# Kernel optimization log

Measured on AMD Instinct MI355X. Metric: run time of the kernel, lower is better.

Reference implementation:

```python
import jax, jax.numpy as jnp
import numpy as np

B, S, DIM, NH, HD = 2, 2048, 4096, 32, 128  # head_dim = dim // n_kv_heads
ROPE_THETA = 10000.0


def _apply_rope(xh, cos, sin):
    # xh: (B, S, H, HD); cos/sin: (S, HD//2). Llama interleaved-pair rotation
    # (view head_dim as complex pairs, multiply by e^{i*theta}).
    b, s, h, d = xh.shape
    xp = xh.reshape(b, s, h, d // 2, 2)
    x0, x1 = xp[..., 0], xp[..., 1]
    c = cos[None, :, None, :]
    sn = sin[None, :, None, :]
    o0 = x0 * c - x1 * sn
    o1 = x0 * sn + x1 * c
    return jnp.stack([o0, o1], axis=-1).reshape(b, s, h, d)


def setup_inputs() -> dict:
    key = jax.random.key(0)
    ks = jax.random.split(key, 5)
    scale = 1.0 / np.sqrt(DIM)
    x = jax.random.normal(ks[0], (B, S, DIM), dtype=jnp.float32)
    wq = jax.random.normal(ks[1], (DIM, DIM), dtype=jnp.float32) * scale
    wk = jax.random.normal(ks[2], (DIM, DIM), dtype=jnp.float32) * scale
    wv = jax.random.normal(ks[3], (DIM, DIM), dtype=jnp.float32) * scale
    wo = jax.random.normal(ks[4], (DIM, DIM), dtype=jnp.float32) * scale
    # precomputed rotary table (real/imag of freqs_cis)
    t = jnp.arange(S, dtype=jnp.float32)
    inv_freq = 1.0 / (ROPE_THETA ** (jnp.arange(0, HD, 2, dtype=jnp.float32) / HD))
    ang = t[:, None] * inv_freq[None, :]  # (S, HD//2)
    freqs_cos, freqs_sin = jnp.cos(ang), jnp.sin(ang)
    # additive causal mask
    i = jnp.arange(S)
    mask = jnp.where(i[None, :] <= i[:, None], 0.0, -jnp.inf).astype(jnp.float32)
    return {"x": x, "wq": wq, "wk": wk, "wv": wv, "wo": wo,
            "freqs_cos": freqs_cos, "freqs_sin": freqs_sin,
            "mask": mask, "start_pos": 0}


def reference(x, wq, wk, wv, wo, freqs_cos, freqs_sin, mask, start_pos):
    bsz, seqlen, dim = x.shape
    # nn.Linear(bias=False): y = x @ W^T
    xq = (x @ wq.T).reshape(bsz, seqlen, NH, HD)
    xk = (x @ wk.T).reshape(bsz, seqlen, NH, HD)
    xv = (x @ wv.T).reshape(bsz, seqlen, NH, HD)
    xq = _apply_rope(xq, freqs_cos, freqs_sin)
    xk = _apply_rope(xk, freqs_cos, freqs_sin)
    # training path: keys/values = current xk/xv (no cache)
    scores = jnp.einsum('bqhd,bkhd->bhqk', xq, xk) / np.sqrt(HD)
    scores = scores + mask[None, None, :, :]
    probs = jax.nn.softmax(scores.astype(jnp.float32), axis=-1).astype(x.dtype)
    out = jnp.einsum('bhqk,bkhd->bqhd', probs, xv).reshape(bsz, seqlen, dim)
    return out @ wo.T
```

## Files before the change

kernel.cpp:

```cpp
#include <hip/hip_runtime.h>

typedef __bf16 bf16;
typedef __attribute__((ext_vector_type(8))) __bf16 bf16x8;
typedef __attribute__((ext_vector_type(4))) float f32x4;

#define MFMA_BF16(a,b,c) __builtin_amdgcn_mfma_f32_16x16x32_bf16((a),(b),(c),0,0,0)

__device__ __forceinline__ void gld_lds16(const void* g, void* l) {
  __builtin_amdgcn_global_load_lds(
      (__attribute__((address_space(1))) void*)(g),
      (__attribute__((address_space(3))) void*)(l), 16, 0, 0);
}

__device__ __forceinline__ bf16x8 cvt8(float4 u, float4 v) {
  bf16x8 r;
  r[0] = (bf16)u.x; r[1] = (bf16)u.y; r[2] = (bf16)u.z; r[3] = (bf16)u.w;
  r[4] = (bf16)v.x; r[5] = (bf16)v.y; r[6] = (bf16)v.z; r[7] = (bf16)v.w;
  return r;
}

__global__ __launch_bounds__(256) void fill_kernel(float* p, int n, float v) {
  int i = blockIdx.x * 256 + threadIdx.x;
  if (i < n) p[i] = v;
}

__global__ __launch_bounds__(256) void cvt_kernel(const float* __restrict__ s, bf16* __restrict__ d) {
  size_t i = ((size_t)blockIdx.x * 256 + threadIdx.x) * 4;
  float4 a = *(const float4*)(s + i);
  ushort4 r;
  r.x = __builtin_bit_cast(unsigned short, (bf16)a.x);
  r.y = __builtin_bit_cast(unsigned short, (bf16)a.y);
  r.z = __builtin_bit_cast(unsigned short, (bf16)a.z);
  r.w = __builtin_bit_cast(unsigned short, (bf16)a.w);
  *(ushort4*)(d + i) = r;
}


template<int IH, int KS>
__device__ __forceinline__ void mfma_phase(const char* rb, int sA, int sB,
                                           f32x4 (&acc)[8][4], bf16x8 (&bq)[4])
{
  bf16x8 afr[4];
#pragma unroll
  for (int i2 = 0; i2 < 4; ++i2)
    afr[i2] = *(const bf16x8*)(rb + KS * 16384 + sA + (IH * 4 + i2) * 1024);
  if (IH == 0) {
#pragma unroll
    for (int j = 0; j < 4; ++j)
      bq[j] = *(const bf16x8*)(rb + 32768 + KS * 16384 + sB + j * 1024);
  }
  __builtin_amdgcn_s_barrier();
  __builtin_amdgcn_s_setprio(1);
#pragma unroll
  for (int i2 = 0; i2 < 4; ++i2)
#pragma unroll
    for (int j = 0; j < 4; ++j)
      acc[IH * 4 + i2][j] = MFMA_BF16(afr[i2], bq[j], acc[IH * 4 + i2][j]);
  __builtin_amdgcn_s_setprio(0);
}

__device__ __forceinline__ void gemm256_core(
    const bf16* __restrict__ Ag, const bf16* __restrict__ Wg,
    char* smem, int m0, int n0, f32x4 (&acc)[8][4])
{
  constexpr int NT = 64;
  const int tid = threadIdx.x;
  const int lane = tid & 63;
  const int l15 = lane & 15, quad = lane >> 4;
  const int wave = tid >> 6;
  const int wm = wave >> 2, wn = wave & 3;

  const int swz = (((l15 & 1) * 4 + quad) ^ (l15 >> 1));
  const int sA = ((wm * 64 + (l15 >> 1)) * 8 + swz) * 16;
  const int sB = ((wn * 32 + (l15 >> 1)) * 8 + swz) * 16;

  int r0, c0, r1, c1;
  { int s = tid;       int rp = s >> 3, y = (s & 7) ^ (rp & 7); r0 = rp * 2 + (y >> 2); c0 = y & 3; }
  { int s = 512 + tid; int rp = s >> 3, y = (s & 7) ^ (rp & 7); r1 = rp * 2 + (y >> 2); c1 = y & 3; }

  const bf16* gA0 = Ag + (size_t)(m0 + r0) * 4096 + c0 * 8;
  const bf16* gA1 = Ag + (size_t)(m0 + r1) * 4096 + c1 * 8;
  const bf16* gB0 = Wg + (size_t)(n0 + r0) * 4096 + c0 * 8;
  const bf16* gB1 = Wg + (size_t)(n0 + r1) * 4096 + c1 * 8;

  const int d0 = tid * 16, d1 = (512 + tid) * 16;

#pragma unroll
  for (int i = 0; i < 8; i++)
#pragma unroll
    for (int j = 0; j < 4; j++) acc[i][j] = (f32x4){0.f, 0.f, 0.f, 0.f};

  gld_lds16(gA0,      smem + d0);          gld_lds16(gA1,      smem + d1);
  gld_lds16(gB0,      smem + 32768 + d0);  gld_lds16(gB1,      smem + 32768 + d1);
  gld_lds16(gA0 + 32, smem + 16384 + d0);  gld_lds16(gA1 + 32, smem + 16384 + d1);
  gld_lds16(gB0 + 32, smem + 49152 + d0);  gld_lds16(gB1 + 32, smem + 49152 + d1);

#pragma unroll 2
  for (int t = 0; t < NT; ++t) {
    const int p = t & 1;
    const char* rb = smem + p * 65536;
    char* wb = smem + (p ^ 1) * 65536;
    const int kn = (t + 1) * 64;
    const bool st = (t + 1 < NT);

    asm volatile("s_waitcnt vmcnt(4)" ::: "memory");
    __builtin_amdgcn_s_barrier();

    bf16x8 bq0[4];
    if (st) { gld_lds16(gA0 + kn, wb + d0); gld_lds16(gA1 + kn, wb + d1); }
    mfma_phase<0, 0>(rb, sA, sB, acc, bq0);
    __builtin_amdgcn_s_barrier();

    if (st) { gld_lds16(gB0 + kn, wb + 32768 + d0); gld_lds16(gB1 + kn, wb + 32768 + d1); }
    mfma_phase<1, 0>(rb, sA, sB, acc, bq0);

    if (st) asm volatile("s_waitcnt vmcnt(4)" ::: "memory");
    else    asm volatile("s_waitcnt vmcnt(0)" ::: "memory");
    __builtin_amdgcn_s_barrier();

    bf16x8 bq1[4];
    if (st) { gld_lds16(gA0 + kn + 32, wb + 16384 + d0); gld_lds16(gA1 + kn + 32, wb + 16384 + d1); }
    mfma_phase<0, 1>(rb, sA, sB, acc, bq1);
    __builtin_amdgcn_s_barrier();

    if (st) { gld_lds16(gB0 + kn + 32, wb + 49152 + d0); gld_lds16(gB1 + kn + 32, wb + 49152 + d1); }
    mfma_phase<1, 1>(rb, sA, sB, acc, bq1);
  }
}

__global__ __launch_bounds__(512) void gemm256_qkv(
    const bf16* __restrict__ A,
    const bf16* __restrict__ W0, const bf16* __restrict__ W1, const bf16* __restrict__ W2,
    bf16* __restrict__ C0, bf16* __restrict__ C1, bf16* __restrict__ C2)
{
  __shared__ __align__(16) char smem[131072];
  const int z = blockIdx.z;
  const bf16* __restrict__ W = (z == 0) ? W0 : ((z == 1) ? W1 : W2);
  bf16* __restrict__ C = (z == 0) ? C0 : ((z == 1) ? C1 : C2);

  const int bid = blockIdx.x;
  const int swb = (bid & 7) * 32 + (bid >> 3);
  const int m0 = (swb & 15) << 8;
  const int n0 = (swb >> 4) << 8;

  f32x4 acc[8][4];
  gemm256_core(A, W, smem, m0, n0, acc);

  const int tid = threadIdx.x, lane = tid & 63, wave = tid >> 6;
  const int l15 = lane & 15, quad = lane >> 4;
  const int wm = wave >> 2, wn = wave & 3;

  if (z == 2) {
#pragma unroll
    for (int i = 0; i < 8; i++) {
      const int mg = m0 + wm * 128 + i * 16 + quad * 4;
      const int bb = mg >> 11, ss = mg & 2047;
#pragma unroll
      for (int j = 0; j < 4; j++) {
        const int n = n0 + wn * 64 + j * 16 + l15;
        ushort4 pk;
        pk.x = __builtin_bit_cast(unsigned short, (bf16)acc[i][j][0]);
        pk.y = __builtin_bit_cast(unsigned short, (bf16)acc[i][j][1]);
        pk.z = __builtin_bit_cast(unsigned short, (bf16)acc[i][j][2]);
        pk.w = __builtin_bit_cast(unsigned short, (bf16)acc[i][j][3]);
        *(ushort4*)&C[((size_t)bb * 4096 + n) * 2048 + ss] = pk;
      }
    }
  } else {
#pragma unroll
    for (int i = 0; i < 8; i++) {
      const int row = m0 + wm * 128 + i * 16 + quad * 4;
#pragma unroll
      for (int j = 0; j < 4; j++) {
        const int col = n0 + wn * 64 + j * 16 + l15;
#pragma unroll
        for (int r = 0; r < 4; r++)
          C[(size_t)(row + r) * 4096 + col] = (bf16)acc[i][j][r];
      }
    }
  }
}

__global__ __launch_bounds__(512) void gemm256_out(
    const bf16* __restrict__ A, const bf16* __restrict__ W, float* __restrict__ C)
{
  __shared__ __align__(16) char smem[131072];
  const int bid = blockIdx.x;
  const int swb = (bid & 7) * 32 + (bid >> 3);
  const int m0 = (swb & 15) << 8;
  const int n0 = (swb >> 4) << 8;

  f32x4 acc[8][4];
  gemm256_core(A, W, smem, m0, n0, acc);

  const int tid = threadIdx.x, lane = tid & 63, wave = tid >> 6;
  const int l15 = lane & 15, quad = lane >> 4;
  const int wm = wave >> 2, wn = wave & 3;

#pragma unroll
  for (int i = 0; i < 8; i++) {
    const int row = m0 + wm * 128 + i * 16 + quad * 4;
#pragma unroll
    for (int j = 0; j < 4; j++) {
      const int col = n0 + wn * 64 + j * 16 + l15;
#pragma unroll
      for (int r = 0; r < 4; r++)
        C[(size_t)(row + r) * 4096 + col] = acc[i][j][r];
    }
  }
}

__global__ __launch_bounds__(256) void gemm_f32in(
    const float* __restrict__ A,
    const float* __restrict__ W0, const float* __restrict__ W1, const float* __restrict__ W2,
    bf16* __restrict__ C0, bf16* __restrict__ C1, bf16* __restrict__ C2)
{
  constexpr int K = 4096, N = 4096;
  __shared__ __align__(16) bf16 As[128 * 32];
  __shared__ __align__(16) bf16 Bs[128 * 32];
  const int z = blockIdx.z;
  const float* __restrict__ W = (z == 0) ? W0 : ((z == 1) ? W1 : W2);
  bf16* __restrict__ C = (z == 0) ? C0 : ((z == 1) ? C1 : C2);
  const int tid = threadIdx.x;
  const int lane = tid & 63, wave = tid >> 6;
  const int l15 = lane & 15, quad = lane >> 4;
  const int m0 = blockIdx.x * 128, n0 = blockIdx.y * 128;
  const int wm = (wave & 1) * 64, wn = (wave >> 1) * 64;

  const int srow = tid >> 2;
  const int scol = (tid & 3) * 8;
  const float* gA = A + (size_t)(m0 + srow) * K + scol;
  const float* gW = W + (size_t)(n0 + srow) * K + scol;
  bf16* lA = &As[srow * 32 + scol];
  bf16* lB = &Bs[srow * 32 + scol];

  f32x4 acc[4][4];
#pragma unroll
  for (int i = 0; i < 4; i++)
#pragma unroll
    for (int j = 0; j < 4; j++) acc[i][j] = (f32x4){0.f, 0.f, 0.f, 0.f};

  for (int k0 = 0; k0 < K; k0 += 32) {
    float4 a0 = *(const float4*)(gA + k0);
    float4 a1 = *(const float4*)(gA + k0 + 4);
    float4 a2 = *(const float4*)(gA + k0 + (size_t)64 * K);
    float4 a3 = *(const float4*)(gA + k0 + (size_t)64 * K + 4);
    float4 b0 = *(const float4*)(gW + k0);
    float4 b1 = *(const float4*)(gW + k0 + 4);
    float4 b2 = *(const float4*)(gW + k0 + (size_t)64 * K);
    float4 b3 = *(const float4*)(gW + k0 + (size_t)64 * K + 4);
    __syncthreads();
    *(bf16x8*)lA              = cvt8(a0, a1);
    *(bf16x8*)(lA + 64 * 32)  = cvt8(a2, a3);
    *(bf16x8*)lB              = cvt8(b0, b1);
    *(bf16x8*)(lB + 64 * 32)  = cvt8(b2, b3);
    __syncthreads();
    bf16x8 af[4], bfr[4];
#pragma unroll
    for (int i = 0; i < 4; i++) af[i]  = *(const bf16x8*)&As[(wm + i * 16 + l15) * 32 + quad * 8];
#pragma unroll
    for (int j = 0; j < 4; j++) bfr[j] = *(const bf16x8*)&Bs[(wn + j * 16 + l15) * 32 + quad * 8];
#pragma unroll
    for (int i = 0; i < 4; i++)
#pragma unroll
      for (int j = 0; j < 4; j++)
        acc[i][j] = MFMA_BF16(af[i], bfr[j], acc[i][j]);
  }

  if (z == 2) {
#pragma unroll
    for (int i = 0; i < 4; i++) {
      const int mg = m0 + wm + i * 16 + quad * 4;
      const int bb = mg >> 11, ss = mg & 2047;
#pragma unroll
      for (int j = 0; j < 4; j++) {
        const int n = n0 + wn + j * 16 + l15;
        ushort4 pk;
        pk.x = __builtin_bit_cast(unsigned short, (bf16)acc[i][j][0]);
        pk.y = __builtin_bit_cast(unsigned short, (bf16)acc[i][j][1]);
        pk.z = __builtin_bit_cast(unsigned short, (bf16)acc[i][j][2]);
        pk.w = __builtin_bit_cast(unsigned short, (bf16)acc[i][j][3]);
        *(ushort4*)&C[((size_t)bb * 4096 + n) * 2048 + ss] = pk;
      }
    }
  } else {
#pragma unroll
    for (int i = 0; i < 4; i++) {
      const int row = m0 + wm + i * 16 + quad * 4;
#pragma unroll
      for (int j = 0; j < 4; j++) {
        const int col = n0 + wn + j * 16 + l15;
#pragma unroll
        for (int r = 0; r < 4; r++)
          C[(size_t)(row + r) * N + col] = (bf16)acc[i][j][r];
      }
    }
  }
}

__global__ __launch_bounds__(256) void rope_kernel(
    bf16* __restrict__ q, bf16* __restrict__ kk,
    const float* __restrict__ fc, const float* __restrict__ fs)
{
  const int t = blockIdx.x * 256 + threadIdx.x;
  const int i4 = (t & 15) << 2;
  const int row = t >> 4;
  const int s = (row >> 5) & 2047;

  float4 c4 = *(const float4*)(fc + s * 64 + i4);
  float4 s4 = *(const float4*)(fs + s * 64 + i4);
  float c[4]  = {c4.x, c4.y, c4.z, c4.w};
  float sn[4] = {s4.x, s4.y, s4.z, s4.w};

  const int off = row * 128 + (i4 << 1);
  uint4 qv = *(const uint4*)(q + off);
  uint4 kv = *(const uint4*)(kk + off);
  unsigned qa[4] = {qv.x, qv.y, qv.z, qv.w};
  unsigned ka[4] = {kv.x, kv.y, kv.z, kv.w};
#pragma unroll
  for (int p = 0; p < 4; p++) {
    float x0 = __builtin_bit_cast(float, (qa[p] & 0xffffu) << 16);
    float x1 = __builtin_bit_cast(float, (qa[p] >> 16) << 16);
    unsigned lo = __builtin_bit_cast(unsigned short, (bf16)(x0 * c[p] - x1 * sn[p]));
    unsigned hi = __builtin_bit_cast(unsigned short, (bf16)(x0 * sn[p] + x1 * c[p]));
    qa[p] = lo | (hi << 16);
    float y0 = __builtin_bit_cast(float, (ka[p] & 0xffffu) << 16);
    float y1 = __builtin_bit_cast(float, (ka[p] >> 16) << 16);
    lo = __builtin_bit_cast(unsigned short, (bf16)(y0 * c[p] - y1 * sn[p]));
    hi = __builtin_bit_cast(unsigned short, (bf16)(y0 * sn[p] + y1 * c[p]));
    ka[p] = lo | (hi << 16);
  }
  *(uint4*)(q + off)  = make_uint4(qa[0], qa[1], qa[2], qa[3]);
  *(uint4*)(kk + off) = make_uint4(ka[0], ka[1], ka[2], ka[3]);
}

__global__ __launch_bounds__(256) void flash_attn(
    const bf16* __restrict__ Kg_, const bf16* __restrict__ VT, bf16* __restrict__ QO)
{
  __shared__ __align__(16) char smem[81920];
  bf16* Qs = (bf16*)smem;
  bf16* Ks = (bf16*)(smem + 16384);
  bf16* Vs = (bf16*)(smem + 49152);

  const int tid = threadIdx.x, lane = tid & 63, wave = tid >> 6;
  const int l15 = lane & 15, quad = lane >> 4;
  const int r7 = l15 & 7;
  const int q0 = blockIdx.x * 64, h = blockIdx.y, b = blockIdx.z;

  bf16* Qg       = QO  + ((size_t)(b * 2048 + q0) * 32 + h) * 128;
  const bf16* Kg = Kg_ + ((size_t)b * 2048 * 32 + h) * 128;
  const bf16* Vg = VT  + ((size_t)(b * 32 + h)) * 128 * 2048;

#pragma unroll
  for (int it = 0; it < 4; ++it) {
    int c = it * 256 + tid;
    int rr = c >> 4, cc = (c & 15) ^ (rr & 7);
    gld_lds16(Qg + (size_t)rr * 4096 + cc * 8, &Qs[c * 8]);
  }
  __syncthreads();
  bf16x8 qf[4];
#pragma unroll
  for (int ks = 0; ks < 4; ks++)
    qf[ks] = *(const bf16x8*)&Qs[(wave * 16 + l15) * 128 + (((ks * 4 + quad) ^ r7) * 8)];

  bf16* Ps = (bf16*)smem + wave * (16 * 136);

  float m_i[4], l_i[4];
  f32x4 oacc[8];
#pragma unroll
  for (int r = 0; r < 4; r++) { m_i[r] = -INFINITY; l_i[r] = 0.f; }
#pragma unroll
  for (int j = 0; j < 8; j++) oacc[j] = (f32x4){0.f, 0.f, 0.f, 0.f};

  const float SCL = 0.08838834764831845f * 1.4426950408889634f;

  const int nct = (blockIdx.x >> 1) + 1;
  for (int ct = 0; ct < nct; ++ct) {
    __syncthreads();
    const bf16* Kt = Kg + (size_t)ct * 128 * 4096;
    const bf16* Vt = Vg + ct * 128;
#pragma unroll
    for (int it = 0; it < 8; ++it) {
      int c = it * 256 + tid;
      int rr = c >> 4, cc = (c & 15) ^ (rr & 7);
      gld_lds16(Kt + (size_t)rr * 4096 + cc * 8, &Ks[c * 8]);
      gld_lds16(Vt + (size_t)rr * 2048 + cc * 8, &Vs[c * 8]);
    }
    __syncthreads();

    f32x4 sacc[8];
#pragma unroll
    for (int nb = 0; nb < 8; nb++) {
      f32x4 a = (f32x4){0.f, 0.f, 0.f, 0.f};
#pragma unroll
      for (int ks = 0; ks < 4; ks++) {
        bf16x8 kf = *(const bf16x8*)&Ks[(nb * 16 + l15) * 128 + (((ks * 4 + quad) ^ r7) * 8)];
        a = MFMA_BF16(qf[ks], kf, a);
      }
      sacc[nb] = a;
    }

    const int qb = q0 + wave * 16 + quad * 4;
    const int kbase = ct * 128 + l15;
    float alpha[4];
#pragma unroll
    for (int r = 0; r < 4; r++) {
      float mx = -INFINITY;
#pragma unroll
      for (int nb = 0; nb < 8; nb++) {
        float s = sacc[nb][r] * SCL;
        if (kbase + nb * 16 > qb + r) s = -INFINITY;
        sacc[nb][r] = s;
        mx = fmaxf(mx, s);
      }
#pragma unroll
      for (int off = 1; off < 16; off <<= 1) mx = fmaxf(mx, __shfl_xor(mx, off));
      float mn = fmaxf(m_i[r], mx);
      alpha[r] = exp2f(m_i[r] - mn);
      m_i[r] = mn;
      float rs = 0.f;
#pragma unroll
      for (int nb = 0; nb < 8; nb++) {
        float p = exp2f(sacc[nb][r] - mn);
        rs += p;
        Ps[(quad * 4 + r) * 136 + nb * 16 + l15] = (bf16)p;
      }
#pragma unroll
      for (int off = 1; off < 16; off <<= 1) rs += __shfl_xor(rs, off);
      l_i[r] = l_i[r] * alpha[r] + rs;
    }
#pragma unroll
    for (int j = 0; j < 8; j++)
#pragma unroll
      for (int r = 0; r < 4; r++) oacc[j][r] *= alpha[r];

    __syncthreads();

#pragma unroll
    for (int ks2 = 0; ks2 < 4; ks2++) {
      bf16x8 pf = *(const bf16x8*)&Ps[l15 * 136 + ks2 * 32 + quad * 8];
#pragma unroll
      for (int j = 0; j < 8; j++) {
        bf16x8 vf = *(const bf16x8*)&Vs[(j * 16 + l15) * 128 + (((ks2 * 4 + quad) ^ r7) * 8)];
        oacc[j] = MFMA_BF16(pf, vf, oacc[j]);
      }
    }
  }

#pragma unroll
  for (int r = 0; r < 4; r++) {
    const float inv = 1.f / l_i[r];
    const int row = q0 + wave * 16 + quad * 4 + r;
    bf16* Og = QO + ((size_t)(b * 2048 + row) * 32 + h) * 128;
#pragma unroll
    for (int j = 0; j < 8; j++) Og[j * 16 + l15] = (bf16)(oacc[j][r] * inv);
  }
}

extern "C" void kernel_launch(void* const* d_in, const int* in_sizes, int n_in,
                              void* d_out, int out_size, void* d_ws, size_t ws_size,
                              hipStream_t stream) {
  const float* x  = (const float*)d_in[0];
  const float* wq = (const float*)d_in[1];
  const float* wk = (const float*)d_in[2];
  const float* wv = (const float*)d_in[3];
  const float* wo = (const float*)d_in[4];
  const float* fc = (const float*)d_in[5];
  const float* fs = (const float*)d_in[6];
  float* out = (float*)d_out;

  float sentinel = 0.f;
  if (n_in < 9 || in_sizes[0] != 16777216) sentinel = 200.f;
  else if (out_size != 16777216)           sentinel = 300.f;
  else if (in_sizes[5] != 131072)          sentinel = 400.f;
  else if (ws_size < 3ull * 33554432ull)   sentinel = 100.f;
  if (sentinel != 0.f) {
    fill_kernel<<<dim3((out_size + 255) / 256), dim3(256), 0, stream>>>(out, out_size, sentinel);
    return;
  }

  bf16* q  = (bf16*)d_ws;
  bf16* k  = q  + (size_t)16777216;
  bf16* vt = k  + (size_t)16777216;

  dim3 blk(256, 1, 1);
  dim3 blk512(512, 1, 1);
  const bool bigws = (ws_size >= 7ull * 33554432ull);

  if (bigws) {
    bf16* xb  = vt  + (size_t)16777216;
    bf16* wqb = xb  + (size_t)16777216;
    bf16* wkb = wqb + (size_t)16777216;
    bf16* wvb = wkb + (size_t)16777216;
    cvt_kernel<<<dim3(16384), blk, 0, stream>>>(x,  xb);
    cvt_kernel<<<dim3(16384), blk, 0, stream>>>(wq, wqb);
    cvt_kernel<<<dim3(16384), blk, 0, stream>>>(wk, wkb);
    cvt_kernel<<<dim3(16384), blk, 0, stream>>>(wv, wvb);
    gemm256_qkv<<<dim3(256, 1, 3), blk512, 0, stream>>>(xb, wqb, wkb, wvb, q, k, vt);
  } else {
    gemm_f32in<<<dim3(32, 32, 3), blk, 0, stream>>>(x, wq, wk, wv, q, k, vt);
  }
  rope_kernel<<<dim3(8192), blk, 0, stream>>>(q, k, fc, fs);
  flash_attn<<<dim3(32, 32, 2), blk, 0, stream>>>(k, vt, q);
  cvt_kernel<<<dim3(16384), blk, 0, stream>>>(wo, k);
  gemm256_out<<<dim3(256, 1, 1), blk512, 0, stream>>>(q, k, out);
}
```

Before: 1.178 ms.

## Deepen GEMM global-to-LDS prefetch to run further ahead of MFMA consumption

Restructures the GEMM main loop so global-to-LDS loads for later k-tiles are issued earlier. Each iteration now stages parts of tiles t+1 and t+2, and waits use a larger vmcnt budget to keep more loads in flight. Two peeled epilogue iterations drain the pipeline. The goal is to hide global memory latency behind the MFMA phases. The cost is more complex buffer-reuse timing within the two LDS buffers, which risks hazards if the waits and barriers do not line up with the slot-reuse order.

```diff
diff --git a/kernel.cpp b/kernel.cpp
--- a/kernel.cpp
+++ b/kernel.cpp
@@ -85,45 +85,80 @@
 
   const int d0 = tid * 16, d1 = (512 + tid) * 16;
 
+  auto stA = [&](int t2, int ks) {
+    char* L = smem + (t2 & 1) * 65536 + ks * 16384;
+    gld_lds16(gA0 + t2 * 64 + ks * 32, L + d0);
+    gld_lds16(gA1 + t2 * 64 + ks * 32, L + d1);
+  };
+  auto stB = [&](int t2, int ks) {
+    char* L = smem + (t2 & 1) * 65536 + 32768 + ks * 16384;
+    gld_lds16(gB0 + t2 * 64 + ks * 32, L + d0);
+    gld_lds16(gB1 + t2 * 64 + ks * 32, L + d1);
+  };
+
 #pragma unroll
   for (int i = 0; i < 8; i++)
 #pragma unroll
     for (int j = 0; j < 4; j++) acc[i][j] = (f32x4){0.f, 0.f, 0.f, 0.f};
 
-  gld_lds16(gA0,      smem + d0);          gld_lds16(gA1,      smem + d1);
-  gld_lds16(gB0,      smem + 32768 + d0);  gld_lds16(gB1,      smem + 32768 + d1);
-  gld_lds16(gA0 + 32, smem + 16384 + d0);  gld_lds16(gA1 + 32, smem + 16384 + d1);
-  gld_lds16(gB0 + 32, smem + 49152 + d0);  gld_lds16(gB1 + 32, smem + 49152 + d1);
+  stB(0, 0); stA(0, 0); stB(0, 1); stA(0, 1); stB(1, 0); stA(1, 0); stB(1, 1);
 
 #pragma unroll 2
-  for (int t = 0; t < NT; ++t) {
-    const int p = t & 1;
-    const char* rb = smem + p * 65536;
-    char* wb = smem + (p ^ 1) * 65536;
-    const int kn = (t + 1) * 64;
-    const bool st = (t + 1 < NT);
-
+  for (int t = 0; t < NT - 2; ++t) {
+    const char* rb = smem + (t & 1) * 65536;
+
+    asm volatile("s_waitcnt vmcnt(10)" ::: "memory");
+    __builtin_amdgcn_s_barrier();
+
+    bf16x8 bq0[4];
+    stA(t + 1, 1);
+    mfma_phase<0, 0>(rb, sA, sB, acc, bq0);
+    __builtin_amdgcn_s_barrier();
+
+    stB(t + 2, 0);
+    mfma_phase<1, 0>(rb, sA, sB, acc, bq0);
+
+    asm volatile("s_waitcnt vmcnt(10)" ::: "memory");
+    __builtin_amdgcn_s_barrier();
+
+    bf16x8 bq1[4];
+    stA(t + 2, 0);
+    mfma_phase<0, 1>(rb, sA, sB, acc, bq1);
+    __builtin_amdgcn_s_barrier();
+
+    stB(t + 2, 1);
+    mfma_phase<1, 1>(rb, sA, sB, acc, bq1);
+  }
+
+  {
+    const char* rb = smem;
+    asm volatile("s_waitcnt vmcnt(10)" ::: "memory");
+    __builtin_amdgcn_s_barrier();
+    bf16x8 bq0[4];
+    stA(NT - 1, 1);
+    mfma_phase<0, 0>(rb, sA, sB, acc, bq0);
+    __builtin_amdgcn_s_barrier();
+    mfma_phase<1, 0>(rb, sA, sB, acc, bq0);
+    asm volatile("s_waitcnt vmcnt(8)" ::: "memory");
+    __builtin_amdgcn_s_barrier();
+    bf16x8 bq1[4];
+    mfma_phase<0, 1>(rb, sA, sB, acc, bq1);
+    __builtin_amdgcn_s_barrier();
+    mfma_phase<1, 1>(rb, sA, sB, acc, bq1);
+  }
+  {
+    const char* rb = smem + 65536;
     asm volatile("s_waitcnt vmcnt(4)" ::: "memory");
     __builtin_amdgcn_s_barrier();
-
     bf16x8 bq0[4];
-    if (st) { gld_lds16(gA0 + kn, wb + d0); gld_lds16(gA1 + kn, wb + d1); }
     mfma_phase<0, 0>(rb, sA, sB, acc, bq0);
     __builtin_amdgcn_s_barrier();
-
-    if (st) { gld_lds16(gB0 + kn, wb + 32768 + d0); gld_lds16(gB1 + kn, wb + 32768 + d1); }
     mfma_phase<1, 0>(rb, sA, sB, acc, bq0);
-
-    if (st) asm volatile("s_waitcnt vmcnt(4)" ::: "memory");
-    else    asm volatile("s_waitcnt vmcnt(0)" ::: "memory");
-    __builtin_amdgcn_s_barrier();
-
+    asm volatile("s_waitcnt vmcnt(0)" ::: "memory");
+    __builtin_amdgcn_s_barrier();
     bf16x8 bq1[4];
-    if (st) { gld_lds16(gA0 + kn + 32, wb + 16384 + d0); gld_lds16(gA1 + kn + 32, wb + 16384 + d1); }
     mfma_phase<0, 1>(rb, sA, sB, acc, bq1);
     __builtin_amdgcn_s_barrier();
-
-    if (st) { gld_lds16(gB0 + kn + 32, wb + 49152 + d0); gld_lds16(gB1 + kn + 32, wb + 49152 + d1); }
     mfma_phase<1, 1>(rb, sA, sB, acc, bq1);
   }
 }
```

After: 1.121 ms. 4.8% less time.
